# Kernel tuning notes

Hardware: AMD Instinct MI355X
Metric: run time of the kernel (lower is better)

## Reference

```python
import jax, jax.numpy as jnp
import numpy as np
import functools

TAU_MEM = 2.0
V_TH = 1.0
V_RESET = 0.0
V_REST = 0.0
DT = 1.0
ALPHA = 2.0  # surrogate sharpness

# atan surrogate: forward = Heaviside, backward = (alpha/2) / (1 + (pi/2*alpha*x)^2)
@jax.custom_vjp
def atan_surrogate(x):
    return (x >= 0).astype(x.dtype)

def _atan_fwd(x):
    return atan_surrogate(x), x

def _atan_bwd(x, g):
    half_pi_alpha = (jnp.pi / 2) * ALPHA
    return (g * (ALPHA / 2) / (1.0 + (half_pi_alpha * x) ** 2),)

atan_surrogate.defvjp(_atan_fwd, _atan_bwd)


def setup_inputs() -> dict:
    key = jax.random.key(0)
    x_seq = jax.random.normal(key, (64, 32, 8192), dtype=jnp.float32)  # (T, B, F)
    return {"x_seq": x_seq}


def reference(x_seq):
    decay = 1.0 / TAU_MEM
    mem0 = jnp.full_like(x_seq[0], V_REST)  # (B, F)

    def step(mem, x):
        mem = mem * (1.0 - decay) + x * DT
        spike = atan_surrogate(mem - V_TH)
        spike_reset = jax.lax.stop_gradient(spike)  # detach_reset=True
        mem = mem * (1.0 - spike_reset) + V_RESET * spike_reset
        return mem, (spike, mem)

    _, (spike_seq, mem_seq) = jax.lax.scan(step, mem0, x_seq)
    return spike_seq, mem_seq
```

## Files before the change

kernel.cpp:

```cpp
#include <hip/hip_runtime.h>
#include <hip/hip_bf16.h>


#define T_STEPS 64
#define BF (32 * 8192)
#define BF2 (BF / 2)

typedef float v2f __attribute__((ext_vector_type(2)));

__global__ __launch_bounds__(256) void lif_fwd_kernel(
    const v2f* __restrict__ x,
    v2f* __restrict__ spike_out,
    v2f* __restrict__ mem_out)
{
    const int idx = blockIdx.x * blockDim.x + threadIdx.x;

    v2f mem = {0.f, 0.f};

#pragma unroll 8
    for (int t = 0; t < T_STEPS; ++t) {
        const v2f xv = __builtin_nontemporal_load(&x[t * BF2 + idx]);

        mem.x = mem.x * 0.5f + xv.x;
        mem.y = mem.y * 0.5f + xv.y;

        v2f sp;
        sp.x = (mem.x >= 1.0f) ? 1.0f : 0.0f;
        sp.y = (mem.y >= 1.0f) ? 1.0f : 0.0f;

        mem.x = (sp.x != 0.0f) ? 0.0f : mem.x;
        mem.y = (sp.y != 0.0f) ? 0.0f : mem.y;

        __builtin_nontemporal_store(sp, &spike_out[t * BF2 + idx]);
        __builtin_nontemporal_store(mem, &mem_out[t * BF2 + idx]);
    }
}

extern "C" void kernel_launch(void* const* d_in, const int* in_sizes, int n_in,
                              void* d_out, int out_size, void* d_ws, size_t ws_size,
                              hipStream_t stream) {
    const v2f* x = (const v2f*)d_in[0];
    v2f* spike_out = (v2f*)d_out;
    v2f* mem_out   = (v2f*)d_out + (size_t)T_STEPS * BF2;

    lif_fwd_kernel<<<BF2 / 256, 256, 0, stream>>>(x, spike_out, mem_out);
}
```

Baseline: 177.0 us.

## Widen to float4 and double-buffer input loads across timestep groups

Each thread now handles four features with 128-bit accesses and explicitly prefetches the next group of 8 timesteps into registers while computing the current group. The aim is more memory-level parallelism per thread, hiding load latency behind the serial membrane recurrence. In exchange the grid is halved, which lowers the wave count per CU, and register pressure rises. The input loads also lose the nontemporal hint.

```diff
diff --git a/kernel.cpp b/kernel.cpp
--- a/kernel.cpp
+++ b/kernel.cpp
@@ -4,44 +4,75 @@
 
 #define T_STEPS 64
 #define BF (32 * 8192)
-#define BF2 (BF / 2)
+#define BF4 (BF / 4)
+#define GRP 8
 
-typedef float v2f __attribute__((ext_vector_type(2)));
+typedef float v4f __attribute__((ext_vector_type(4)));
 
 __global__ __launch_bounds__(256) void lif_fwd_kernel(
-    const v2f* __restrict__ x,
-    v2f* __restrict__ spike_out,
-    v2f* __restrict__ mem_out)
+    const v4f* __restrict__ x,
+    v4f* __restrict__ spike_out,
+    v4f* __restrict__ mem_out)
 {
     const int idx = blockIdx.x * blockDim.x + threadIdx.x;
+    const v4f* xp = x + idx;
+    v4f* so = spike_out + idx;
+    v4f* mo = mem_out + idx;
 
-    v2f mem = {0.f, 0.f};
+    v4f mem = {0.f, 0.f, 0.f, 0.f};
+    v4f buf[2][GRP];
 
-#pragma unroll 8
-    for (int t = 0; t < T_STEPS; ++t) {
-        const v2f xv = __builtin_nontemporal_load(&x[t * BF2 + idx]);
+#pragma unroll
+    for (int j = 0; j < GRP; ++j)
+        buf[0][j] = xp[(size_t)j * BF4];
 
-        mem.x = mem.x * 0.5f + xv.x;
-        mem.y = mem.y * 0.5f + xv.y;
+#pragma unroll
+    for (int g = 0; g < T_STEPS / GRP; ++g) {
+        const int cur = g & 1;
+        const int nxt = cur ^ 1;
 
-        v2f sp;
-        sp.x = (mem.x >= 1.0f) ? 1.0f : 0.0f;
-        sp.y = (mem.y >= 1.0f) ? 1.0f : 0.0f;
+        if (g + 1 < T_STEPS / GRP) {
+#pragma unroll
+            for (int j = 0; j < GRP; ++j)
+                buf[nxt][j] = xp[(size_t)((g + 1) * GRP + j) * BF4];
+        }
 
-        mem.x = (sp.x != 0.0f) ? 0.0f : mem.x;
-        mem.y = (sp.y != 0.0f) ? 0.0f : mem.y;
+#pragma unroll
+        for (int j = 0; j < GRP; ++j) {
+            const int t = g * GRP + j;
+            const v4f xv = buf[cur][j];
 
-        __builtin_nontemporal_store(sp, &spike_out[t * BF2 + idx]);
-        __builtin_nontemporal_store(mem, &mem_out[t * BF2 + idx]);
+            v4f m;
+            m.x = mem.x * 0.5f + xv.x;
+            m.y = mem.y * 0.5f + xv.y;
+            m.z = mem.z * 0.5f + xv.z;
+            m.w = mem.w * 0.5f + xv.w;
+
+            v4f sp;
+            sp.x = (m.x >= 1.0f) ? 1.0f : 0.0f;
+            sp.y = (m.y >= 1.0f) ? 1.0f : 0.0f;
+            sp.z = (m.z >= 1.0f) ? 1.0f : 0.0f;
+            sp.w = (m.w >= 1.0f) ? 1.0f : 0.0f;
+
+            m.x = (sp.x != 0.0f) ? 0.0f : m.x;
+            m.y = (sp.y != 0.0f) ? 0.0f : m.y;
+            m.z = (sp.z != 0.0f) ? 0.0f : m.z;
+            m.w = (sp.w != 0.0f) ? 0.0f : m.w;
+
+            mem = m;
+
+            __builtin_nontemporal_store(sp, &so[(size_t)t * BF4]);
+            __builtin_nontemporal_store(m,  &mo[(size_t)t * BF4]);
+        }
     }
 }
 
 extern "C" void kernel_launch(void* const* d_in, const int* in_sizes, int n_in,
                               void* d_out, int out_size, void* d_ws, size_t ws_size,
                               hipStream_t stream) {
-    const v2f* x = (const v2f*)d_in[0];
-    v2f* spike_out = (v2f*)d_out;
-    v2f* mem_out   = (v2f*)d_out + (size_t)T_STEPS * BF2;
+    const v4f* x = (const v4f*)d_in[0];
+    v4f* spike_out = (v4f*)d_out;
+    v4f* mem_out   = (v4f*)d_out + (size_t)T_STEPS * BF4;
 
-    lif_fwd_kernel<<<BF2 / 256, 256, 0, stream>>>(x, spike_out, mem_out);
+    lif_fwd_kernel<<<BF4 / 256, 256, 0, stream>>>(x, spike_out, mem_out);
 }
```

Result: no change. 178.5 us (+0.9%).
